# Kernel optimization log

Measured on AMD Instinct MI355X. Metric: run time of the kernel, lower is better.

## Reference

```python
import jax, jax.numpy as jnp
import numpy as np

N_SRC = 100000
N_DST = 50000
N_EDGES = 600000
D = 128


def setup_inputs() -> dict:
    key = jax.random.key(0)
    k1, k2, k3, k4, k5 = jax.random.split(key, 5)
    src_rep = jax.random.normal(k1, (N_SRC, D), dtype=jnp.float32)
    dst_rep = jax.random.normal(k2, (N_DST, D), dtype=jnp.float32)
    edge_src = jax.random.randint(k3, (N_EDGES,), 0, N_SRC, dtype=jnp.int64)
    edge_dst = jax.random.randint(k4, (N_EDGES,), 0, N_DST, dtype=jnp.int64)
    W = jax.random.normal(k5, (2 * D, D), dtype=jnp.float32) * (1.0 / np.sqrt(2 * D))
    b = jnp.zeros((D,), dtype=jnp.float32)
    return {"src_rep": src_rep, "dst_rep": dst_rep, "edge_src": edge_src,
            "edge_dst": edge_dst, "W": W, "b": b}


def reference(src_rep, dst_rep, edge_src, edge_dst, W, b):
    # copy_src: gather source reps along edges  [E, D]
    msgs = src_rep[edge_src]
    # sum reduce: scatter-add messages to destination nodes  [N_dst, D]
    agg = jax.ops.segment_sum(msgs, edge_dst, num_segments=dst_rep.shape[0])
    # NodeUpdater: concat(dst rep, summed messages) -> Linear -> activation
    # (Dropout is identity in eval mode.)
    concat = jnp.concatenate([dst_rep, agg], axis=1)  # [N_dst, 2D]
    new_rep = jax.nn.relu(concat @ W + b)  # [N_dst, D]
    return new_rep
```

## Files before the change

kernel.cpp:

```cpp
#include <hip/hip_runtime.h>

#define N_SRC   100000
#define N_DST   50000
#define N_EDGES 600000
#define D       128
#define RPB     16
#define PAD     48

#define CONV_BLOCKS  ((N_SRC * D / 4) / 256)
#define MISC_ELEMS   (2 * D * D + N_DST)
#define MISC_BLOCKS  ((MISC_ELEMS + 255) / 256)
#define FILL_BLOCKS  ((N_EDGES + 255) / 256)

typedef short bf16x8 __attribute__((ext_vector_type(8)));
typedef float f32x4  __attribute__((ext_vector_type(4)));

static __device__ __forceinline__ unsigned short f2bf(float f) {
    unsigned u = __float_as_uint(f);
    u += 0x7FFF + ((u >> 16) & 1);
    return (unsigned short)(u >> 16);
}
static __device__ __forceinline__ unsigned pk(float a, float b) {
    return (unsigned)f2bf(a) | ((unsigned)f2bf(b) << 16);
}
static __device__ __forceinline__ void addpk(float* a, uint4 u) {
    a[0] += __uint_as_float(u.x << 16);
    a[1] += __uint_as_float(u.x & 0xFFFF0000u);
    a[2] += __uint_as_float(u.y << 16);
    a[3] += __uint_as_float(u.y & 0xFFFF0000u);
    a[4] += __uint_as_float(u.z << 16);
    a[5] += __uint_as_float(u.z & 0xFFFF0000u);
    a[6] += __uint_as_float(u.w << 16);
    a[7] += __uint_as_float(u.w & 0xFFFF0000u);
}

__global__ __launch_bounds__(256) void prep_kernel(
    const float* __restrict__ src_rep, unsigned short* __restrict__ srcb,
    const float* __restrict__ W, unsigned short* __restrict__ Wt,
    int* __restrict__ cnt) {
    if (blockIdx.x < CONV_BLOCKS) {
        size_t t = (size_t)blockIdx.x * 256 + threadIdx.x;
        float4 v = reinterpret_cast<const float4*>(src_rep)[t];
        uint2 w;
        w.x = pk(v.x, v.y); w.y = pk(v.z, v.w);
        reinterpret_cast<uint2*>(srcb)[t] = w;
    } else {
        int t = (blockIdx.x - CONV_BLOCKS) * 256 + threadIdx.x;
        if (t < 2 * D * D) {
            int n = t >> 8, k = t & 255;
            Wt[n * 256 + k] = f2bf(W[(size_t)k * D + n]);
        }
        int c = t - 2 * D * D;
        if (c >= 0 && c < N_DST) cnt[c] = 0;
    }
}

__global__ __launch_bounds__(256) void fill_kernel(
    const int* __restrict__ edge_src, const int* __restrict__ edge_dst,
    int* __restrict__ cnt, int* __restrict__ perm) {
    int e = blockIdx.x * 256 + threadIdx.x;
    if (e < N_EDGES) {
        int d = edge_dst[e];
        int pos = atomicAdd(&cnt[d], 1);
        if (pos < PAD) perm[d * PAD + pos] = edge_src[e];
    }
}

__global__ __launch_bounds__(512) void fused_kernel(
    const unsigned short* __restrict__ srcb,
    const float* __restrict__ dst_rep,
    const int*   __restrict__ cnt,
    const int*   __restrict__ perm,
    const unsigned short* __restrict__ Wt,
    const float* __restrict__ bias,
    float*       __restrict__ out) {
    __shared__ unsigned short Abf[16 * 2 * D];
    const int row0 = blockIdx.x * 16;
    const int tid = threadIdx.x, lane = tid & 63, wave = tid >> 6;
    const int q = lane >> 4, cl = lane & 15;

    if (tid < 256) {
        int r = tid >> 4, b = tid & 15;
        const float4* p = reinterpret_cast<const float4*>(
            dst_rep + (size_t)(row0 + r) * D + b * 8);
        float4 v0 = p[0], v1 = p[1];
        uint4 w;
        w.x = pk(v0.x, v0.y); w.y = pk(v0.z, v0.w);
        w.z = pk(v1.x, v1.y); w.w = pk(v1.z, v1.w);
        *reinterpret_cast<uint4*>(&Abf[r * 256 + (b ^ (r & 7)) * 8]) = w;
    }

#pragma unroll
    for (int rr = 0; rr < 2; ++rr) {
        const int r  = wave * 2 + rr;
        const int dn = row0 + r;
        const int deg = min(cnt[dn], PAD);
        const int pi = perm[(size_t)dn * PAD + min(lane, PAD - 1)];
        const int dm1 = deg - 1;
        float a0[8] = {0,0,0,0,0,0,0,0}, a1[8] = {0,0,0,0,0,0,0,0};
        for (int base = 0; base < deg; base += 16) {
            int e0 = base + q, e1 = base + 4 + q, e2 = base + 8 + q, e3 = base + 12 + q;
            int s0 = __shfl(pi, min(e0, dm1));
            int s1 = __shfl(pi, min(e1, dm1));
            int s2 = __shfl(pi, min(e2, dm1));
            int s3 = __shfl(pi, min(e3, dm1));
            uint4 u0 = {0,0,0,0}, u1 = {0,0,0,0}, u2 = {0,0,0,0}, u3 = {0,0,0,0};
            if (e0 <= dm1) u0 = *reinterpret_cast<const uint4*>(srcb + (size_t)s0 * D + cl * 8);
            if (e1 <= dm1) u1 = *reinterpret_cast<const uint4*>(srcb + (size_t)s1 * D + cl * 8);
            if (e2 <= dm1) u2 = *reinterpret_cast<const uint4*>(srcb + (size_t)s2 * D + cl * 8);
            if (e3 <= dm1) u3 = *reinterpret_cast<const uint4*>(srcb + (size_t)s3 * D + cl * 8);
            addpk(a0, u0); addpk(a1, u1); addpk(a0, u2); addpk(a1, u3);
        }
#pragma unroll
        for (int i = 0; i < 8; ++i) {
            a0[i] += a1[i];
            a0[i] += __shfl_xor(a0[i], 16);
            a0[i] += __shfl_xor(a0[i], 32);
        }
        if (lane < 16) {
            uint4 w;
            w.x = pk(a0[0], a0[1]); w.y = pk(a0[2], a0[3]);
            w.z = pk(a0[4], a0[5]); w.w = pk(a0[6], a0[7]);
            *reinterpret_cast<uint4*>(&Abf[r * 256 + ((16 + cl) ^ (r & 7)) * 8]) = w;
        }
    }
    __syncthreads();

    f32x4 c0 = {0.f, 0.f, 0.f, 0.f};
    const int ar = lane & 15;
    const int kb = lane >> 4;
    const int n0 = wave * 16 + (lane & 15);
#pragma unroll
    for (int s = 0; s < 8; ++s) {
        int b = s * 4 + kb;
        bf16x8 af = *reinterpret_cast<const bf16x8*>(&Abf[ar * 256 + (b ^ (ar & 7)) * 8]);
        bf16x8 b0 = *reinterpret_cast<const bf16x8*>(&Wt[(size_t)n0 * 256 + s * 32 + kb * 8]);
        c0 = __builtin_amdgcn_mfma_f32_16x16x32_bf16(af, b0, c0, 0, 0, 0);
    }

    const float bv = bias[n0];
#pragma unroll
    for (int g = 0; g < 4; ++g) {
        size_t orow = row0 + (lane >> 4) * 4 + g;
        out[orow * D + n0] = fmaxf(c0[g] + bv, 0.f);
    }
}

__global__ __launch_bounds__(256) void prep_small_kernel(
    const float* __restrict__ W, unsigned short* __restrict__ Wt,
    int* __restrict__ cnt) {
    int t = blockIdx.x * 256 + threadIdx.x;
    if (t < 2 * D * D) {
        int n = t >> 8, k = t & 255;
        Wt[n * 256 + k] = f2bf(W[(size_t)k * D + n]);
    }
    int c = t - 2 * D * D;
    if (c >= 0 && c < N_DST) cnt[c] = 0;
}

__global__ __launch_bounds__(256) void gather_f32_kernel(
    const float* __restrict__ src_rep,
    const int*   __restrict__ cnt,
    const int*   __restrict__ perm,
    unsigned short* __restrict__ agg) {
    const int tid = threadIdx.x, lane = tid & 63, wave = tid >> 6;
    const int h = lane >> 5, c = lane & 31;
    const int dn = blockIdx.x * 4 + wave;
    const int deg = min(cnt[dn], PAD);
    const int pi = perm[(size_t)dn * PAD + min(lane, PAD - 1)];

    f32x4 a0 = {0.f, 0.f, 0.f, 0.f}, a1 = a0, a2 = a0, a3 = a0;
    const int dm1 = deg - 1;
    for (int base = 0; base < deg; base += 8) {
        int e0 = base + h, e1 = base + 2 + h, e2 = base + 4 + h, e3 = base + 6 + h;
        int s0 = __shfl(pi, min(e0, dm1));
        int s1 = __shfl(pi, min(e1, dm1));
        int s2 = __shfl(pi, min(e2, dm1));
        int s3 = __shfl(pi, min(e3, dm1));
        if (e0 <= dm1) a0 += *reinterpret_cast<const f32x4*>(src_rep + (size_t)s0 * D + c * 4);
        if (e1 <= dm1) a1 += *reinterpret_cast<const f32x4*>(src_rep + (size_t)s1 * D + c * 4);
        if (e2 <= dm1) a2 += *reinterpret_cast<const f32x4*>(src_rep + (size_t)s2 * D + c * 4);
        if (e3 <= dm1) a3 += *reinterpret_cast<const f32x4*>(src_rep + (size_t)s3 * D + c * 4);
    }
    a0 += a1; a2 += a3; a0 += a2;
#pragma unroll
    for (int qq = 0; qq < 4; ++qq) a0[qq] += __shfl_xor(a0[qq], 32);
    if (h == 0) {
        uint2 w;
        w.x = pk(a0[0], a0[1]); w.y = pk(a0[2], a0[3]);
        *reinterpret_cast<uint2*>(agg + (size_t)dn * D + c * 4) = w;
    }
}

__global__ __launch_bounds__(256) void gemm_kernel(
    const float* __restrict__ dst_rep,
    const unsigned short* __restrict__ agg,
    const unsigned short* __restrict__ Wt,
    const float* __restrict__ bias,
    float*       __restrict__ out) {
    __shared__ unsigned short Abf[RPB * 2 * D];
    const int row0 = blockIdx.x * RPB;
    const int tid = threadIdx.x, lane = tid & 63, wave = tid >> 6;
    {
        int r = tid >> 4, b = tid & 15;
        const float4* p = reinterpret_cast<const float4*>(
            dst_rep + (size_t)(row0 + r) * D + b * 8);
        float4 v0 = p[0], v1 = p[1];
        uint4 w;
        w.x = pk(v0.x, v0.y); w.y = pk(v0.z, v0.w);
        w.z = pk(v1.x, v1.y); w.w = pk(v1.z, v1.w);
        *reinterpret_cast<uint4*>(&Abf[r * 256 + (b ^ (r & 7)) * 8]) = w;
        uint4 g = *reinterpret_cast<const uint4*>(agg + (size_t)(row0 + r) * D + b * 8);
        *reinterpret_cast<uint4*>(&Abf[r * 256 + ((16 + b) ^ (r & 7)) * 8]) = g;
    }
    __syncthreads();

    f32x4 c0 = {0.f, 0.f, 0.f, 0.f}, c1 = {0.f, 0.f, 0.f, 0.f};
    const int ar = lane & 15;
    const int kb = lane >> 4;
    const int n0 = wave * 32 + (lane & 15);
#pragma unroll
    for (int s = 0; s < 8; ++s) {
        int b = s * 4 + kb;
        bf16x8 af = *reinterpret_cast<const bf16x8*>(&Abf[ar * 256 + (b ^ (ar & 7)) * 8]);
        int kbase = s * 32 + kb * 8;
        bf16x8 b0 = *reinterpret_cast<const bf16x8*>(&Wt[(size_t)n0 * 256 + kbase]);
        bf16x8 b1 = *reinterpret_cast<const bf16x8*>(&Wt[(size_t)(n0 + 16) * 256 + kbase]);
        c0 = __builtin_amdgcn_mfma_f32_16x16x32_bf16(af, b0, c0, 0, 0, 0);
        c1 = __builtin_amdgcn_mfma_f32_16x16x32_bf16(af, b1, c1, 0, 0, 0);
    }
    const float bv0 = bias[wave * 32 + (lane & 15)];
    const float bv1 = bias[wave * 32 + 16 + (lane & 15)];
#pragma unroll
    for (int g = 0; g < 4; ++g) {
        size_t orow = row0 + (lane >> 4) * 4 + g;
        out[orow * D + wave * 32 + (lane & 15)]      = fmaxf(c0[g] + bv0, 0.f);
        out[orow * D + wave * 32 + 16 + (lane & 15)] = fmaxf(c1[g] + bv1, 0.f);
    }
}

extern "C" void kernel_launch(void* const* d_in, const int* in_sizes, int n_in,
                              void* d_out, int out_size, void* d_ws, size_t ws_size,
                              hipStream_t stream) {
    const float* src_rep  = (const float*)d_in[0];
    const float* dst_rep  = (const float*)d_in[1];
    const int*   edge_src = (const int*)d_in[2];
    const int*   edge_dst = (const int*)d_in[3];
    const float* W        = (const float*)d_in[4];
    const float* bias     = (const float*)d_in[5];
    float*       out      = (float*)d_out;

    int* cnt  = (int*)d_ws;
    int* perm = cnt + N_DST;
    size_t wt_off = (((size_t)N_DST * (1 + PAD) * 4 + 255) / 256) * 256;
    unsigned short* Wt   = (unsigned short*)((char*)d_ws + wt_off);
    unsigned short* big  = Wt + (size_t)2 * D * D;
    const size_t need_full = wt_off + ((size_t)2 * D * D + (size_t)N_SRC * D)
                             * sizeof(unsigned short);

    if (ws_size >= need_full) {
        unsigned short* srcb = big;
        prep_kernel<<<CONV_BLOCKS + MISC_BLOCKS, 256, 0, stream>>>(
            src_rep, srcb, W, Wt, cnt);
        fill_kernel<<<FILL_BLOCKS, 256, 0, stream>>>(edge_src, edge_dst, cnt, perm);
        fused_kernel<<<N_DST / 16, 512, 0, stream>>>(
            srcb, dst_rep, cnt, perm, Wt, bias, out);
    } else {
        unsigned short* agg = big;
        prep_small_kernel<<<MISC_BLOCKS, 256, 0, stream>>>(W, Wt, cnt);
        fill_kernel<<<FILL_BLOCKS, 256, 0, stream>>>(edge_src, edge_dst, cnt, perm);
        gather_f32_kernel<<<N_DST / 4, 256, 0, stream>>>(src_rep, cnt, perm, agg);
        gemm_kernel<<<N_DST / RPB, 256, 0, stream>>>(dst_rep, agg, Wt, bias, out);
    }
}
```

Before: 98.20 us.

## Halve fused kernel block size, process four rows per wave in the gather

The fused gather+GEMM kernel now runs 256 threads per block instead of 512. Each wave gathers four destination rows at once, interleaving their source-row loads across the edge loop, and computes two 16-column MFMA tiles in the GEMM. This gives more independent loads in flight per wave and amortizes the Wt fragment loads, but uses more accumulator registers and iterates up to the maximum degree of the four rows. A max(dm,0) clamp is also added to the shuffle indices for zero-degree rows.

```diff
diff --git a/kernel.cpp b/kernel.cpp
--- a/kernel.cpp
+++ b/kernel.cpp
@@ -66,7 +66,7 @@
     }
 }
 
-__global__ __launch_bounds__(512) void fused_kernel(
+__global__ __launch_bounds__(256) void fused_kernel(
     const unsigned short* __restrict__ srcb,
     const float* __restrict__ dst_rep,
     const int*   __restrict__ cnt,
@@ -79,7 +79,7 @@
     const int tid = threadIdx.x, lane = tid & 63, wave = tid >> 6;
     const int q = lane >> 4, cl = lane & 15;
 
-    if (tid < 256) {
+    {
         int r = tid >> 4, b = tid & 15;
         const float4* p = reinterpret_cast<const float4*>(
             dst_rep + (size_t)(row0 + r) * D + b * 8);
@@ -90,59 +90,68 @@
         *reinterpret_cast<uint4*>(&Abf[r * 256 + (b ^ (r & 7)) * 8]) = w;
     }
 
-#pragma unroll
-    for (int rr = 0; rr < 2; ++rr) {
-        const int r  = wave * 2 + rr;
-        const int dn = row0 + r;
-        const int deg = min(cnt[dn], PAD);
-        const int pi = perm[(size_t)dn * PAD + min(lane, PAD - 1)];
-        const int dm1 = deg - 1;
-        float a0[8] = {0,0,0,0,0,0,0,0}, a1[8] = {0,0,0,0,0,0,0,0};
-        for (int base = 0; base < deg; base += 16) {
-            int e0 = base + q, e1 = base + 4 + q, e2 = base + 8 + q, e3 = base + 12 + q;
-            int s0 = __shfl(pi, min(e0, dm1));
-            int s1 = __shfl(pi, min(e1, dm1));
-            int s2 = __shfl(pi, min(e2, dm1));
-            int s3 = __shfl(pi, min(e3, dm1));
-            uint4 u0 = {0,0,0,0}, u1 = {0,0,0,0}, u2 = {0,0,0,0}, u3 = {0,0,0,0};
-            if (e0 <= dm1) u0 = *reinterpret_cast<const uint4*>(srcb + (size_t)s0 * D + cl * 8);
-            if (e1 <= dm1) u1 = *reinterpret_cast<const uint4*>(srcb + (size_t)s1 * D + cl * 8);
-            if (e2 <= dm1) u2 = *reinterpret_cast<const uint4*>(srcb + (size_t)s2 * D + cl * 8);
-            if (e3 <= dm1) u3 = *reinterpret_cast<const uint4*>(srcb + (size_t)s3 * D + cl * 8);
-            addpk(a0, u0); addpk(a1, u1); addpk(a0, u2); addpk(a1, u3);
-        }
+    const int dn0 = row0 + wave * 4;
+    const int4 c4 = *reinterpret_cast<const int4*>(&cnt[dn0]);
+    int deg[4] = {min(c4.x, PAD), min(c4.y, PAD), min(c4.z, PAD), min(c4.w, PAD)};
+    int pi[4];
+#pragma unroll
+    for (int r = 0; r < 4; ++r)
+        pi[r] = perm[(size_t)(dn0 + r) * PAD + min(lane, PAD - 1)];
+    const int umax = max(max(deg[0], deg[1]), max(deg[2], deg[3]));
+
+    float acc[4][8] = {};
+    for (int base = 0; base < umax; base += 4) {
+        const int e = base + q;
+#pragma unroll
+        for (int r = 0; r < 4; ++r) {
+            int dm = deg[r] - 1;
+            int s = __shfl(pi[r], min(e, max(dm, 0)));
+            if (e <= dm) {
+                uint4 u = *reinterpret_cast<const uint4*>(srcb + (size_t)s * D + cl * 8);
+                addpk(acc[r], u);
+            }
+        }
+    }
+
+#pragma unroll
+    for (int r = 0; r < 4; ++r) {
 #pragma unroll
         for (int i = 0; i < 8; ++i) {
-            a0[i] += a1[i];
-            a0[i] += __shfl_xor(a0[i], 16);
-            a0[i] += __shfl_xor(a0[i], 32);
+            acc[r][i] += __shfl_xor(acc[r][i], 16);
+            acc[r][i] += __shfl_xor(acc[r][i], 32);
         }
         if (lane < 16) {
+            const int rr = wave * 4 + r;
             uint4 w;
-            w.x = pk(a0[0], a0[1]); w.y = pk(a0[2], a0[3]);
-            w.z = pk(a0[4], a0[5]); w.w = pk(a0[6], a0[7]);
-            *reinterpret_cast<uint4*>(&Abf[r * 256 + ((16 + cl) ^ (r & 7)) * 8]) = w;
+            w.x = pk(acc[r][0], acc[r][1]); w.y = pk(acc[r][2], acc[r][3]);
+            w.z = pk(acc[r][4], acc[r][5]); w.w = pk(acc[r][6], acc[r][7]);
+            *reinterpret_cast<uint4*>(&Abf[rr * 256 + ((16 + cl) ^ (rr & 7)) * 8]) = w;
         }
     }
     __syncthreads();
 
-    f32x4 c0 = {0.f, 0.f, 0.f, 0.f};
+    f32x4 c0 = {0.f, 0.f, 0.f, 0.f}, c1 = {0.f, 0.f, 0.f, 0.f};
     const int ar = lane & 15;
     const int kb = lane >> 4;
-    const int n0 = wave * 16 + (lane & 15);
+    const int n0 = wave * 32 + (lane & 15);
 #pragma unroll
     for (int s = 0; s < 8; ++s) {
         int b = s * 4 + kb;
         bf16x8 af = *reinterpret_cast<const bf16x8*>(&Abf[ar * 256 + (b ^ (ar & 7)) * 8]);
-        bf16x8 b0 = *reinterpret_cast<const bf16x8*>(&Wt[(size_t)n0 * 256 + s * 32 + kb * 8]);
+        int kbase = s * 32 + kb * 8;
+        bf16x8 b0 = *reinterpret_cast<const bf16x8*>(&Wt[(size_t)n0 * 256 + kbase]);
+        bf16x8 b1 = *reinterpret_cast<const bf16x8*>(&Wt[(size_t)(n0 + 16) * 256 + kbase]);
         c0 = __builtin_amdgcn_mfma_f32_16x16x32_bf16(af, b0, c0, 0, 0, 0);
-    }
-
-    const float bv = bias[n0];
+        c1 = __builtin_amdgcn_mfma_f32_16x16x32_bf16(af, b1, c1, 0, 0, 0);
+    }
+
+    const float bv0 = bias[n0];
+    const float bv1 = bias[n0 + 16];
 #pragma unroll
     for (int g = 0; g < 4; ++g) {
         size_t orow = row0 + (lane >> 4) * 4 + g;
-        out[orow * D + n0] = fmaxf(c0[g] + bv, 0.f);
+        out[orow * D + n0]      = fmaxf(c0[g] + bv0, 0.f);
+        out[orow * D + n0 + 16] = fmaxf(c1[g] + bv1, 0.f);
     }
 }
 
@@ -173,10 +182,10 @@
     const int dm1 = deg - 1;
     for (int base = 0; base < deg; base += 8) {
         int e0 = base + h, e1 = base + 2 + h, e2 = base + 4 + h, e3 = base + 6 + h;
-        int s0 = __shfl(pi, min(e0, dm1));
-        int s1 = __shfl(pi, min(e1, dm1));
-        int s2 = __shfl(pi, min(e2, dm1));
-        int s3 = __shfl(pi, min(e3, dm1));
+        int s0 = __shfl(pi, min(e0, max(dm1, 0)));
+        int s1 = __shfl(pi, min(e1, max(dm1, 0)));
+        int s2 = __shfl(pi, min(e2, max(dm1, 0)));
+        int s3 = __shfl(pi, min(e3, max(dm1, 0)));
         if (e0 <= dm1) a0 += *reinterpret_cast<const f32x4*>(src_rep + (size_t)s0 * D + c * 4);
         if (e1 <= dm1) a1 += *reinterpret_cast<const f32x4*>(src_rep + (size_t)s1 * D + c * 4);
         if (e2 <= dm1) a2 += *reinterpret_cast<const f32x4*>(src_rep + (size_t)s2 * D + c * 4);
@@ -263,7 +272,7 @@
         prep_kernel<<<CONV_BLOCKS + MISC_BLOCKS, 256, 0, stream>>>(
             src_rep, srcb, W, Wt, cnt);
         fill_kernel<<<FILL_BLOCKS, 256, 0, stream>>>(edge_src, edge_dst, cnt, perm);
-        fused_kernel<<<N_DST / 16, 512, 0, stream>>>(
+        fused_kernel<<<N_DST / 16, 256, 0, stream>>>(
             srcb, dst_rep, cnt, perm, Wt, bias, out);
     } else {
         unsigned short* agg = big;
```

New measurement: 107.2 us. 1.09x slower.
